# Optimization experiments

Hardware: AMD Instinct MI355X
Metric: run time of the kernel (lower is better)

## Reference

```python
import jax, jax.numpy as jnp
import numpy as np

N, B, E = 50000, 1, 800000
D_IN = 128      # input_size == out_size (residual)
HID = 128       # hidden_size
H = 4           # heads
C = HID // H    # per-head dim = 32
EPS = 1e-5


def setup_inputs() -> dict:
    key = jax.random.key(0)
    ks = jax.random.split(key, 16)
    s_in = 1.0 / np.sqrt(D_IN)
    s_hid = 1.0 / np.sqrt(HID)
    return {
        "x": jax.random.normal(ks[0], (N, B, D_IN), jnp.float32),
        "edge_index": jax.random.randint(ks[1], (2, E), 0, N, jnp.int64 if jax.config.jax_enable_x64 else jnp.int32),
        "edge_attr": jax.random.normal(ks[2], (E, HID), jnp.float32),
        # TransformerConv projections (weights stored torch-style [out, in])
        "Wq": jax.random.uniform(ks[3], (HID, D_IN), jnp.float32, -s_in, s_in),
        "bq": jnp.zeros((HID,), jnp.float32),
        "Wk": jax.random.uniform(ks[4], (HID, D_IN), jnp.float32, -s_in, s_in),
        "bk": jnp.zeros((HID,), jnp.float32),
        "Wv": jax.random.uniform(ks[5], (HID, D_IN), jnp.float32, -s_in, s_in),
        "bv": jnp.zeros((HID,), jnp.float32),
        "We": jax.random.uniform(ks[6], (HID, HID), jnp.float32, -s_hid, s_hid),  # lin_edge, no bias
        "Wskip": jax.random.uniform(ks[7], (HID, D_IN), jnp.float32, -s_in, s_in),
        "bskip": jnp.zeros((HID,), jnp.float32),
        "Wp": jax.random.uniform(ks[8], (HID, HID), jnp.float32, -s_hid, s_hid),   # physics_linear
        "bp": jnp.zeros((HID,), jnp.float32),
        "Wm": jax.random.uniform(ks[9], (D_IN, HID), jnp.float32, -s_hid, s_hid),  # merge_linear
        "bm": jnp.zeros((D_IN,), jnp.float32),
    }


def reference(x, edge_index, edge_attr, Wq, bq, Wk, bk, Wv, bv, We,
              Wskip, bskip, Wp, bp, Wm, bm):
    n = x.shape[0]
    src, dst = edge_index[0], edge_index[1]  # message flows src -> dst (j -> i)

    # node-wise QKV projections -> [N, B, H, C]
    q = (x @ Wq.T + bq).reshape(n, B, H, C)
    k = (x @ Wk.T + bk).reshape(n, B, H, C)
    v = (x @ Wv.T + bv).reshape(n, B, H, C)

    # edge feature projection -> [E, H, C]
    e = (edge_attr @ We.T).reshape(-1, H, C)

    # per-edge attention scores [E, B, H]
    k_j = k[src] + e[:, None]                       # [E, B, H, C]
    alpha = (q[dst] * k_j).sum(-1) / jnp.sqrt(jnp.asarray(C, x.dtype))

    # scatter-softmax over incoming edges of each dst node
    m = jax.ops.segment_max(alpha, dst, num_segments=n)      # [N, B, H]
    a = jnp.exp(alpha - m[dst])
    s = jax.ops.segment_sum(a, dst, num_segments=n)
    alpha = a / s[dst]

    # weighted scatter-add aggregation
    msg = (v[src] + e[:, None]) * alpha[..., None]           # [E, B, H, C]
    out = jax.ops.segment_sum(msg, dst, num_segments=n)      # [N, B, H, C]
    out = out.reshape(n, B, H * C)

    # root skip connection
    out = out + (x @ Wskip.T + bskip)

    # GraphResidualBlock tail
    out = jax.nn.relu(out)
    out = out @ Wp.T + bp
    # custom LayerNorm: normalize over the node dim (dim 0), weight/bias unused
    mu = out.mean(0, keepdims=True)
    sd = out.std(0, keepdims=True)
    out = (out - mu) / (sd + EPS)
    out = jax.nn.relu(out)
    out = out @ Wm.T + bm
    return out + x
```

## Files before the change

kernel.cpp:

```cpp
#include <hip/hip_runtime.h>
#include <stdint.h>

#define RS32 0.17677669529663687f
#define LDW 40

typedef short bf16x8 __attribute__((ext_vector_type(8)));
typedef float f32x4 __attribute__((ext_vector_type(4)));

__device__ __forceinline__ ushort f2bf(float f) {
  uint32_t b = __float_as_uint(f);
  b = (b + 0x7fffu + ((b >> 16) & 1u)) >> 16;
  return (ushort)b;
}
__device__ __forceinline__ float bflo(uint32_t w) { return __uint_as_float(w << 16); }
__device__ __forceinline__ float bfhi(uint32_t w) { return __uint_as_float(w & 0xffff0000u); }

__device__ __forceinline__ void stage16(ushort* hiA, ushort* loA, int r, int koff,
                                        const float* v) {
  uint32_t hu[8], lu[8];
#pragma unroll
  for (int i = 0; i < 8; ++i) {
    ushort h0 = f2bf(v[2 * i]), h1 = f2bf(v[2 * i + 1]);
    float f0 = __uint_as_float(((uint32_t)h0) << 16);
    float f1 = __uint_as_float(((uint32_t)h1) << 16);
    ushort l0 = f2bf(v[2 * i] - f0), l1 = f2bf(v[2 * i + 1] - f1);
    hu[i] = (uint32_t)h0 | ((uint32_t)h1 << 16);
    lu[i] = (uint32_t)l0 | ((uint32_t)l1 << 16);
  }
  *(uint4*)&hiA[r * LDW + koff]     = make_uint4(hu[0], hu[1], hu[2], hu[3]);
  *(uint4*)&hiA[r * LDW + koff + 8] = make_uint4(hu[4], hu[5], hu[6], hu[7]);
  *(uint4*)&loA[r * LDW + koff]     = make_uint4(lu[0], lu[1], lu[2], lu[3]);
  *(uint4*)&loA[r * LDW + koff + 8] = make_uint4(lu[4], lu[5], lu[6], lu[7]);
}

__launch_bounds__(256)
__global__ void gemm128_mfma_kernel(int mode,
                                    const float* __restrict__ A, const float* __restrict__ A2,
                                    const float* __restrict__ W, const float* __restrict__ bias,
                                    const float* __restrict__ mu, const float* __restrict__ inv,
                                    const float* __restrict__ X, float* __restrict__ out, int N)
{
  __shared__ ushort Ahi[128 * LDW], Alo[128 * LDW], Whi[128 * LDW], Wlo[128 * LDW];
  const int tid = threadIdx.x;
  const int nb = blockIdx.x * 128;
  const int lane = tid & 63, wv = tid >> 6;
  const int wr = (wv >> 1) * 64, wc = (wv & 1) * 64;
  const int fr = lane & 15, fq = lane >> 4;
  const int sr = tid >> 1, sk = (tid & 1) * 16;

  f32x4 acc[4][4];
#pragma unroll
  for (int m = 0; m < 4; ++m)
#pragma unroll
    for (int n = 0; n < 4; ++n) acc[m][n] = (f32x4)0.0f;

  for (int kc = 0; kc < 128; kc += 32) {
    float va[16], vw[16];
    {
      int gr = nb + sr;
      if (gr < N) {
#pragma unroll
        for (int i = 0; i < 4; ++i) {
          float4 v = *(const float4*)(A + (size_t)gr * 128 + kc + sk + i * 4);
          if (mode == 1) {
            float4 b = *(const float4*)(A2 + (size_t)gr * 128 + kc + sk + i * 4);
            v.x = fmaxf(v.x + b.x, 0.f); v.y = fmaxf(v.y + b.y, 0.f);
            v.z = fmaxf(v.z + b.z, 0.f); v.w = fmaxf(v.w + b.w, 0.f);
          } else if (mode == 2) {
            float4 m4 = *(const float4*)(mu + kc + sk + i * 4);
            float4 i4 = *(const float4*)(inv + kc + sk + i * 4);
            v.x = fmaxf((v.x - m4.x) * i4.x, 0.f); v.y = fmaxf((v.y - m4.y) * i4.y, 0.f);
            v.z = fmaxf((v.z - m4.z) * i4.z, 0.f); v.w = fmaxf((v.w - m4.w) * i4.w, 0.f);
          }
          va[i * 4 + 0] = v.x; va[i * 4 + 1] = v.y; va[i * 4 + 2] = v.z; va[i * 4 + 3] = v.w;
        }
      } else {
#pragma unroll
        for (int i = 0; i < 16; ++i) va[i] = 0.f;
      }
#pragma unroll
      for (int i = 0; i < 4; ++i) {
        float4 v = *(const float4*)(W + (size_t)sr * 128 + kc + sk + i * 4);
        vw[i * 4 + 0] = v.x; vw[i * 4 + 1] = v.y; vw[i * 4 + 2] = v.z; vw[i * 4 + 3] = v.w;
      }
    }
    if (kc) __syncthreads();
    stage16(Ahi, Alo, sr, sk, va);
    stage16(Whi, Wlo, sr, sk, vw);
    __syncthreads();

    bf16x8 ah[4], al[4], bh[4], bl[4];
#pragma unroll
    for (int m = 0; m < 4; ++m) {
      const int row = wr + m * 16 + fr;
      ah[m] = *(const bf16x8*)&Ahi[row * LDW + fq * 8];
      al[m] = *(const bf16x8*)&Alo[row * LDW + fq * 8];
    }
#pragma unroll
    for (int n = 0; n < 4; ++n) {
      const int col = wc + n * 16 + fr;
      bh[n] = *(const bf16x8*)&Whi[col * LDW + fq * 8];
      bl[n] = *(const bf16x8*)&Wlo[col * LDW + fq * 8];
    }
#pragma unroll
    for (int m = 0; m < 4; ++m)
#pragma unroll
      for (int n = 0; n < 4; ++n) {
        acc[m][n] = __builtin_amdgcn_mfma_f32_16x16x32_bf16(ah[m], bh[n], acc[m][n], 0, 0, 0);
        acc[m][n] = __builtin_amdgcn_mfma_f32_16x16x32_bf16(al[m], bh[n], acc[m][n], 0, 0, 0);
        acc[m][n] = __builtin_amdgcn_mfma_f32_16x16x32_bf16(ah[m], bl[n], acc[m][n], 0, 0, 0);
      }
  }

  float bcol[4];
#pragma unroll
  for (int n = 0; n < 4; ++n) bcol[n] = bias[wc + n * 16 + fr];
#pragma unroll
  for (int m = 0; m < 4; ++m) {
    const int r0 = nb + wr + m * 16 + fq * 4;
#pragma unroll
    for (int r = 0; r < 4; ++r) {
      const int gr = r0 + r;
      if (gr < N) {
#pragma unroll
        for (int n = 0; n < 4; ++n) {
          const int c = wc + n * 16 + fr;
          float o = acc[m][n][r] + bcol[n];
          if (mode == 2) o += X[(size_t)gr * 128 + c];
          out[(size_t)gr * 128 + c] = o;
        }
      }
    }
  }
}

__launch_bounds__(256)
__global__ void gemmqkvs_mfma_kernel(const float* __restrict__ x,
                                     const float* __restrict__ Wq, const float* __restrict__ bq,
                                     const float* __restrict__ Wk, const float* __restrict__ bk,
                                     const float* __restrict__ Wv, const float* __restrict__ bv,
                                     const float* __restrict__ Ws, const float* __restrict__ bs,
                                     float* __restrict__ oq, float* __restrict__ ok,
                                     float* __restrict__ ov, float* __restrict__ os, int N)
{
  const float* W; const float* bias; float* out;
  if (blockIdx.y == 0)      { W = Wq; bias = bq; out = oq; }
  else if (blockIdx.y == 1) { W = Wk; bias = bk; out = ok; }
  else if (blockIdx.y == 2) { W = Wv; bias = bv; out = ov; }
  else                      { W = Ws; bias = bs; out = os; }

  __shared__ ushort Ahi[128 * LDW], Alo[128 * LDW], Whi[128 * LDW], Wlo[128 * LDW];
  const int tid = threadIdx.x;
  const int nb = blockIdx.x * 128;
  const int lane = tid & 63, wv = tid >> 6;
  const int wr = (wv >> 1) * 64, wc = (wv & 1) * 64;
  const int fr = lane & 15, fq = lane >> 4;
  const int sr = tid >> 1, sk = (tid & 1) * 16;

  f32x4 acc[4][4];
#pragma unroll
  for (int m = 0; m < 4; ++m)
#pragma unroll
    for (int n = 0; n < 4; ++n) acc[m][n] = (f32x4)0.0f;

  for (int kc = 0; kc < 128; kc += 32) {
    float va[16], vw[16];
    {
      int gr = nb + sr;
      if (gr < N) {
#pragma unroll
        for (int i = 0; i < 4; ++i) {
          float4 v = *(const float4*)(x + (size_t)gr * 128 + kc + sk + i * 4);
          va[i * 4 + 0] = v.x; va[i * 4 + 1] = v.y; va[i * 4 + 2] = v.z; va[i * 4 + 3] = v.w;
        }
      } else {
#pragma unroll
        for (int i = 0; i < 16; ++i) va[i] = 0.f;
      }
#pragma unroll
      for (int i = 0; i < 4; ++i) {
        float4 v = *(const float4*)(W + (size_t)sr * 128 + kc + sk + i * 4);
        vw[i * 4 + 0] = v.x; vw[i * 4 + 1] = v.y; vw[i * 4 + 2] = v.z; vw[i * 4 + 3] = v.w;
      }
    }
    if (kc) __syncthreads();
    stage16(Ahi, Alo, sr, sk, va);
    stage16(Whi, Wlo, sr, sk, vw);
    __syncthreads();

    bf16x8 ah[4], al[4], bh[4], bl[4];
#pragma unroll
    for (int m = 0; m < 4; ++m) {
      const int row = wr + m * 16 + fr;
      ah[m] = *(const bf16x8*)&Ahi[row * LDW + fq * 8];
      al[m] = *(const bf16x8*)&Alo[row * LDW + fq * 8];
    }
#pragma unroll
    for (int n = 0; n < 4; ++n) {
      const int col = wc + n * 16 + fr;
      bh[n] = *(const bf16x8*)&Whi[col * LDW + fq * 8];
      bl[n] = *(const bf16x8*)&Wlo[col * LDW + fq * 8];
    }
#pragma unroll
    for (int m = 0; m < 4; ++m)
#pragma unroll
      for (int n = 0; n < 4; ++n) {
        acc[m][n] = __builtin_amdgcn_mfma_f32_16x16x32_bf16(ah[m], bh[n], acc[m][n], 0, 0, 0);
        acc[m][n] = __builtin_amdgcn_mfma_f32_16x16x32_bf16(al[m], bh[n], acc[m][n], 0, 0, 0);
        acc[m][n] = __builtin_amdgcn_mfma_f32_16x16x32_bf16(ah[m], bl[n], acc[m][n], 0, 0, 0);
      }
  }

  float bcol[4];
#pragma unroll
  for (int n = 0; n < 4; ++n) bcol[n] = bias[wc + n * 16 + fr];
#pragma unroll
  for (int m = 0; m < 4; ++m) {
    const int r0 = nb + wr + m * 16 + fq * 4;
#pragma unroll
    for (int r = 0; r < 4; ++r) {
      const int gr = r0 + r;
      if (gr < N) {
#pragma unroll
        for (int n = 0; n < 4; ++n) {
          const int c = wc + n * 16 + fr;
          out[(size_t)gr * 128 + c] = acc[m][n][r] + bcol[n];
        }
      }
    }
  }
}

__launch_bounds__(256)
__global__ void u_kernel(const float* __restrict__ q, const float* __restrict__ We,
                         ushort* __restrict__ u, int N)
{
  __shared__ float qs[64][128];
  const int tid = threadIdx.x;
  const int nb = blockIdx.x * 64;
  for (int idx = tid; idx < 64 * 128; idx += 256) {
    int r = idx >> 7, kk = idx & 127;
    qs[r][kk] = (nb + r < N) ? q[(size_t)(nb + r) * 128 + kk] : 0.f;
  }
  __syncthreads();
  const int j = tid & 127, half = tid >> 7;
  for (int h = 0; h < 4; ++h) {
    float w[32];
#pragma unroll
    for (int c = 0; c < 32; ++c) w[c] = We[(size_t)(32 * h + c) * 128 + j];
    for (int nn = half; nn < 64; nn += 2) {
      float acc = 0.f;
#pragma unroll
      for (int c4 = 0; c4 < 32; c4 += 4) {
        float4 qq = *(const float4*)&qs[nn][32 * h + c4];
        acc = fmaf(qq.x, w[c4], acc);
        acc = fmaf(qq.y, w[c4 + 1], acc);
        acc = fmaf(qq.z, w[c4 + 2], acc);
        acc = fmaf(qq.w, w[c4 + 3], acc);
      }
      int gr = nb + nn;
      if (gr < N) u[(size_t)gr * 512 + h * 128 + j] = f2bf(acc);
    }
  }
}

__global__ void prep_web_kernel(const float* __restrict__ We, ushort* __restrict__ WeB)
{
  int idx = blockIdx.x * 256 + threadIdx.x;
  if (idx >= 128 * 512) return;
  int c = idx >> 9, j = idx & 511;
  int hh = j >> 7, k2 = j & 127;
  WeB[idx] = (hh == (c >> 5)) ? f2bf(We[(size_t)c * 128 + k2]) : (ushort)0;
}

__global__ void deg_kernel(const int* __restrict__ ei, int* __restrict__ deg, int E)
{
  int e = blockIdx.x * 256 + threadIdx.x;
  if (e < E) atomicAdd(&deg[ei[E + e]], 1);
}

__launch_bounds__(256)
__global__ void start_kernel(const int* __restrict__ deg, int* __restrict__ offs,
                             int* __restrict__ cursor, int* __restrict__ gcount, int N)
{
  const int i = blockIdx.x * 256 + threadIdx.x;
  const int lane = threadIdx.x & 63;
  int d = (i < N) ? deg[i] : 0;
  int scan = d;
#pragma unroll
  for (int ofs = 1; ofs < 64; ofs <<= 1) {
    int t = __shfl_up(scan, ofs, 64);
    if (lane >= ofs) scan += t;
  }
  int total = __shfl(scan, 63, 64);
  int base = 0;
  if (lane == 63) base = atomicAdd(gcount, total);
  base = __shfl(base, 63, 64);
  int excl = base + scan - d;
  if (i < N) { offs[i] = excl; cursor[i] = excl; }
}

__global__ void fill_kernel(const int* __restrict__ ei, int* __restrict__ cursor,
                            int2* __restrict__ csr, int E)
{
  int e = blockIdx.x * 256 + threadIdx.x;
  if (e < E) {
    int dst = ei[E + e];
    int slot = atomicAdd(&cursor[dst], 1);
    csr[slot] = make_int2(ei[e], e);
  }
}

__launch_bounds__(256)
__global__ void fused_attn2_kernel(const int2* __restrict__ csr, const int* __restrict__ offs,
                                   const int* __restrict__ deg,
                                   const float* __restrict__ q, const float* __restrict__ kbuf,
                                   const float* __restrict__ vbuf, const ushort* __restrict__ u,
                                   const float* __restrict__ eattr,
                                   ushort* __restrict__ aggS, float* __restrict__ wsS, int N)
{
  const int tid = threadIdx.x;
  const int lane = tid & 63;
  const int wid = tid >> 6;
  const int p = lane >> 5;
  const int j32 = lane & 31;
  const int c0 = j32 * 4;
  const int h = j32 >> 3;
  const int gwave = blockIdx.x * 4 + wid;
  const int nwaves = gridDim.x * 4;

  for (int n = gwave; n < N; n += nwaves) {
    const int e0 = offs[n];
    const int e1 = e0 + deg[n];

    const float4 qv = *(const float4*)(q + (size_t)n * 128 + c0);
    float uh[4][4];
#pragma unroll
    for (int hh = 0; hh < 4; ++hh) {
      uint2 U = *(const uint2*)(u + (size_t)n * 512 + hh * 128 + c0);
      uh[hh][0] = bflo(U.x); uh[hh][1] = bfhi(U.x);
      uh[hh][2] = bflo(U.y); uh[hh][3] = bfhi(U.y);
    }

    float ws0 = 0.f, ws1 = 0.f, ws2 = 0.f, ws3 = 0.f;
    float ax[4][4];
#pragma unroll
    for (int hh = 0; hh < 4; ++hh)
#pragma unroll
      for (int j = 0; j < 4; ++j) ax[hh][j] = 0.f;
    float sm0 = 0.f, sm1 = 0.f, sm2 = 0.f, sm3 = 0.f;

    int sl = e0 + p;
    if (sl < e1) {
      int2 seC = csr[sl];
      float4 eaC = *(const float4*)(eattr + (size_t)seC.y * 128 + c0);
      float4 kC  = *(const float4*)(kbuf + (size_t)seC.x * 128 + c0);
      float4 vC  = *(const float4*)(vbuf + (size_t)seC.x * 128 + c0);
      int sln = sl + 2;
      int2 seN = (sln < e1) ? csr[sln] : seC;
      for (; sl < e1; sl += 2) {
        float4 eaN = *(const float4*)(eattr + (size_t)seN.y * 128 + c0);
        float4 kN  = *(const float4*)(kbuf + (size_t)seN.x * 128 + c0);
        float4 vN  = *(const float4*)(vbuf + (size_t)seN.x * 128 + c0);
        const int slf = sl + 4;
        int2 seF = (slf < e1) ? csr[slf] : seN;

        float P0 = eaC.x * uh[0][0] + eaC.y * uh[0][1] + eaC.z * uh[0][2] + eaC.w * uh[0][3];
        float P1 = eaC.x * uh[1][0] + eaC.y * uh[1][1] + eaC.z * uh[1][2] + eaC.w * uh[1][3];
        float P2 = eaC.x * uh[2][0] + eaC.y * uh[2][1] + eaC.z * uh[2][2] + eaC.w * uh[2][3];
        float P3 = eaC.x * uh[3][0] + eaC.y * uh[3][1] + eaC.z * uh[3][2] + eaC.w * uh[3][3];
        const float qk = qv.x * kC.x + qv.y * kC.y + qv.z * kC.z + qv.w * kC.w;
        P0 += (h == 0) ? qk : 0.f;
        P1 += (h == 1) ? qk : 0.f;
        P2 += (h == 2) ? qk : 0.f;
        P3 += (h == 3) ? qk : 0.f;
#pragma unroll
        for (int mm = 1; mm <= 16; mm <<= 1) {
          P0 += __shfl_xor(P0, mm, 64);
          P1 += __shfl_xor(P1, mm, 64);
          P2 += __shfl_xor(P2, mm, 64);
          P3 += __shfl_xor(P3, mm, 64);
        }
        const float a0 = __expf(P0 * RS32);
        const float a1 = __expf(P1 * RS32);
        const float a2 = __expf(P2 * RS32);
        const float a3 = __expf(P3 * RS32);
        sm0 += a0; sm1 += a1; sm2 += a2; sm3 += a3;
        const float aV = (h == 0) ? a0 : (h == 1) ? a1 : (h == 2) ? a2 : a3;
        ws0 = fmaf(aV, vC.x, ws0); ws1 = fmaf(aV, vC.y, ws1);
        ws2 = fmaf(aV, vC.z, ws2); ws3 = fmaf(aV, vC.w, ws3);
        ax[0][0] = fmaf(a0, eaC.x, ax[0][0]); ax[0][1] = fmaf(a0, eaC.y, ax[0][1]);
        ax[0][2] = fmaf(a0, eaC.z, ax[0][2]); ax[0][3] = fmaf(a0, eaC.w, ax[0][3]);
        ax[1][0] = fmaf(a1, eaC.x, ax[1][0]); ax[1][1] = fmaf(a1, eaC.y, ax[1][1]);
        ax[1][2] = fmaf(a1, eaC.z, ax[1][2]); ax[1][3] = fmaf(a1, eaC.w, ax[1][3]);
        ax[2][0] = fmaf(a2, eaC.x, ax[2][0]); ax[2][1] = fmaf(a2, eaC.y, ax[2][1]);
        ax[2][2] = fmaf(a2, eaC.z, ax[2][2]); ax[2][3] = fmaf(a2, eaC.w, ax[2][3]);
        ax[3][0] = fmaf(a3, eaC.x, ax[3][0]); ax[3][1] = fmaf(a3, eaC.y, ax[3][1]);
        ax[3][2] = fmaf(a3, eaC.z, ax[3][2]); ax[3][3] = fmaf(a3, eaC.w, ax[3][3]);

        eaC = eaN; kC = kN; vC = vN; seN = seF;
      }
    }

#pragma unroll
    for (int hh = 0; hh < 4; ++hh)
#pragma unroll
      for (int j = 0; j < 4; ++j) ax[hh][j] += __shfl_xor(ax[hh][j], 32, 64);
    ws0 += __shfl_xor(ws0, 32, 64); ws1 += __shfl_xor(ws1, 32, 64);
    ws2 += __shfl_xor(ws2, 32, 64); ws3 += __shfl_xor(ws3, 32, 64);
    sm0 += __shfl_xor(sm0, 32, 64); sm1 += __shfl_xor(sm1, 32, 64);
    sm2 += __shfl_xor(sm2, 32, 64); sm3 += __shfl_xor(sm3, 32, 64);

    const float iv0 = (sm0 > 0.f) ? 1.f / sm0 : 0.f;
    const float iv1 = (sm1 > 0.f) ? 1.f / sm1 : 0.f;
    const float iv2 = (sm2 > 0.f) ? 1.f / sm2 : 0.f;
    const float iv3 = (sm3 > 0.f) ? 1.f / sm3 : 0.f;

    if (p == 0) {
      const float s = (h == 0) ? iv0 : (h == 1) ? iv1 : (h == 2) ? iv2 : iv3;
      *(float4*)(wsS + (size_t)n * 128 + c0) =
          make_float4(ws0 * s, ws1 * s, ws2 * s, ws3 * s);
    }

    float o0[4], o1[4], s0, s1;
    if (p == 0) {
#pragma unroll
      for (int j = 0; j < 4; ++j) { o0[j] = ax[0][j]; o1[j] = ax[1][j]; }
      s0 = iv0; s1 = iv1;
    } else {
#pragma unroll
      for (int j = 0; j < 4; ++j) { o0[j] = ax[2][j]; o1[j] = ax[3][j]; }
      s0 = iv2; s1 = iv3;
    }
    uint2 w0 = make_uint2(((uint32_t)f2bf(o0[0] * s0)) | (((uint32_t)f2bf(o0[1] * s0)) << 16),
                          ((uint32_t)f2bf(o0[2] * s0)) | (((uint32_t)f2bf(o0[3] * s0)) << 16));
    uint2 w1 = make_uint2(((uint32_t)f2bf(o1[0] * s1)) | (((uint32_t)f2bf(o1[1] * s1)) << 16),
                          ((uint32_t)f2bf(o1[2] * s1)) | (((uint32_t)f2bf(o1[3] * s1)) << 16));
    *(uint2*)(aggS + (size_t)n * 512 + (p * 2) * 128 + c0) = w0;
    *(uint2*)(aggS + (size_t)n * 512 + (p * 2 + 1) * 128 + c0) = w1;
  }
}

__launch_bounds__(256)
__global__ void agg_gemm_kernel(const ushort* __restrict__ aggS, const ushort* __restrict__ WeB,
                                const float* __restrict__ wsX, float* __restrict__ attn, int N)
{
  __shared__ ushort As[128][72];
  __shared__ ushort Bs[128][72];
  const int tid = threadIdx.x;
  const int nb = blockIdx.x * 128;
  const int lane = tid & 63, wv = tid >> 6;
  const int wr = (wv >> 1) * 64, wc = (wv & 1) * 64;
  const int fr = lane & 15, fq = lane >> 4;
  const int r = tid >> 1, cs = (tid & 1) * 32;

  f32x4 acc[4][4];
#pragma unroll
  for (int m = 0; m < 4; ++m)
#pragma unroll
    for (int n = 0; n < 4; ++n) acc[m][n] = (f32x4)0.0f;

  for (int kc = 0; kc < 512; kc += 64) {
    uint4 av[4], bv[4];
    if (nb + r < N) {
      const uint4* src = (const uint4*)(aggS + (size_t)(nb + r) * 512 + kc + cs);
      av[0] = src[0]; av[1] = src[1]; av[2] = src[2]; av[3] = src[3];
    } else {
#pragma unroll
      for (int i = 0; i < 4; ++i) av[i] = make_uint4(0, 0, 0, 0);
    }
    {
      const uint4* src = (const uint4*)(WeB + (size_t)r * 512 + kc + cs);
      bv[0] = src[0]; bv[1] = src[1]; bv[2] = src[2]; bv[3] = src[3];
    }
    if (kc) __syncthreads();
#pragma unroll
    for (int i = 0; i < 4; ++i) {
      *(uint4*)&As[r][cs + i * 8] = av[i];
      *(uint4*)&Bs[r][cs + i * 8] = bv[i];
    }
    __syncthreads();

#pragma unroll
    for (int s = 0; s < 2; ++s) {
      bf16x8 ah[4], bh[4];
#pragma unroll
      for (int m = 0; m < 4; ++m)
        ah[m] = *(const bf16x8*)&As[wr + m * 16 + fr][s * 32 + fq * 8];
#pragma unroll
      for (int n = 0; n < 4; ++n)
        bh[n] = *(const bf16x8*)&Bs[wc + n * 16 + fr][s * 32 + fq * 8];
#pragma unroll
      for (int m = 0; m < 4; ++m)
#pragma unroll
        for (int n = 0; n < 4; ++n)
          acc[m][n] = __builtin_amdgcn_mfma_f32_16x16x32_bf16(ah[m], bh[n], acc[m][n], 0, 0, 0);
    }
  }

#pragma unroll
  for (int m = 0; m < 4; ++m) {
    const int r0 = nb + wr + m * 16 + fq * 4;
#pragma unroll
    for (int rr = 0; rr < 4; ++rr) {
      const int gr = r0 + rr;
      if (gr < N) {
#pragma unroll
        for (int n = 0; n < 4; ++n) {
          const int c = wc + n * 16 + fr;
          attn[(size_t)gr * 128 + c] = acc[m][n][rr] + wsX[(size_t)gr * 128 + c];
        }
      }
    }
  }
}

__launch_bounds__(256)
__global__ void stats_kernel(const float* __restrict__ t1, float* __restrict__ sums,
                             float* __restrict__ sumsq, int N)
{
  const int tid = threadIdx.x;
  const int c = tid & 127, half = tid >> 7;
  float s = 0.f, s2 = 0.f;
  for (int r = blockIdx.x * 2 + half; r < N; r += gridDim.x * 2) {
    float vv = t1[(size_t)r * 128 + c];
    s += vv; s2 = fmaf(vv, vv, s2);
  }
  __shared__ float ls[256], ls2[256];
  ls[tid] = s; ls2[tid] = s2;
  __syncthreads();
  if (tid < 128) {
    atomicAdd(&sums[c], ls[tid] + ls[tid + 128]);
    atomicAdd(&sumsq[c], ls2[tid] + ls2[tid + 128]);
  }
}

__global__ void finalize_stats_kernel(const float* __restrict__ sums, const float* __restrict__ sumsq,
                                      float* __restrict__ mu, float* __restrict__ inv, int N)
{
  int c = threadIdx.x;
  float m = sums[c] / (float)N;
  float var = sumsq[c] / (float)N - m * m;
  float sd = sqrtf(fmaxf(var, 0.f));
  mu[c] = m;
  inv[c] = 1.f / (sd + 1e-5f);
}

extern "C" void kernel_launch(void* const* d_in, const int* in_sizes, int n_in,
                              void* d_out, int out_size, void* d_ws, size_t ws_size,
                              hipStream_t stream) {
  const float* x    = (const float*)d_in[0];
  const int*   ei   = (const int*)d_in[1];
  const float* eatt = (const float*)d_in[2];
  const float* Wq = (const float*)d_in[3];  const float* bq = (const float*)d_in[4];
  const float* Wk = (const float*)d_in[5];  const float* bk = (const float*)d_in[6];
  const float* Wv = (const float*)d_in[7];  const float* bv = (const float*)d_in[8];
  const float* We = (const float*)d_in[9];
  const float* Wsk = (const float*)d_in[10]; const float* bsk = (const float*)d_in[11];
  const float* Wp = (const float*)d_in[12]; const float* bp = (const float*)d_in[13];
  const float* Wm = (const float*)d_in[14]; const float* bm = (const float*)d_in[15];
  float* out = (float*)d_out;

  const int N = in_sizes[0] / 128;
  const int E = in_sizes[1] / 2;

  char* w = (char*)d_ws;
  auto alloc = [&](size_t bytes) {
    char* p = w;
    w += (bytes + 255) & ~(size_t)255;
    return p;
  };
  const size_t node_f = (size_t)N * 128 * sizeof(float);
  float*  q    = (float*)alloc(node_f);
  float*  kk   = (float*)alloc(node_f);
  float*  vv   = (float*)alloc(node_f);
  float*  skip = (float*)alloc(node_f);
  float*  wsA  = (float*)alloc(node_f);
  ushort* u    = (ushort*)alloc((size_t)N * 512 * sizeof(ushort));
  ushort* aggS = (ushort*)alloc((size_t)N * 512 * sizeof(ushort));
  ushort* WeB  = (ushort*)alloc(128 * 512 * sizeof(ushort));
  int*    deg  = (int*)alloc((size_t)N * sizeof(int));
  int*    offs = (int*)alloc((size_t)N * sizeof(int));
  int*    curs = (int*)alloc((size_t)N * sizeof(int));
  int*    gcnt = (int*)alloc(sizeof(int));
  int2*   csr  = (int2*)alloc((size_t)E * sizeof(int2));
  float*  sums  = (float*)alloc(128 * sizeof(float));
  float*  sumsq = (float*)alloc(128 * sizeof(float));
  float*  mu    = (float*)alloc(128 * sizeof(float));
  float*  inv   = (float*)alloc(128 * sizeof(float));
  float*  t1   = q;
  (void)ws_size; (void)n_in; (void)out_size;

  const int NB = (N + 127) / 128;
  const int EB = (E + 255) / 256;

  hipMemsetAsync(deg, 0, (size_t)N * sizeof(int), stream);
  hipMemsetAsync(gcnt, 0, sizeof(int), stream);
  hipMemsetAsync(sums, 0, 2 * 128 * sizeof(float), stream);

  gemmqkvs_mfma_kernel<<<dim3(NB, 4), 256, 0, stream>>>(x, Wq, bq, Wk, bk, Wv, bv, Wsk, bsk,
                                                        q, kk, vv, skip, N);
  u_kernel<<<(N + 63) / 64, 256, 0, stream>>>(q, We, u, N);
  prep_web_kernel<<<256, 256, 0, stream>>>(We, WeB);

  deg_kernel<<<EB, 256, 0, stream>>>(ei, deg, E);
  start_kernel<<<(N + 255) / 256, 256, 0, stream>>>(deg, offs, curs, gcnt, N);
  fill_kernel<<<EB, 256, 0, stream>>>(ei, curs, csr, E);

  fused_attn2_kernel<<<2048, 256, 0, stream>>>(csr, offs, deg, q, kk, vv, u, eatt,
                                               aggS, wsA, N);

  agg_gemm_kernel<<<NB, 256, 0, stream>>>(aggS, WeB, wsA, wsA, N);

  gemm128_mfma_kernel<<<NB, 256, 0, stream>>>(1, wsA, skip, Wp, bp, nullptr, nullptr, nullptr, t1, N);

  stats_kernel<<<256, 256, 0, stream>>>(t1, sums, sumsq, N);
  finalize_stats_kernel<<<1, 128, 0, stream>>>(sums, sumsq, mu, inv, N);

  gemm128_mfma_kernel<<<NB, 256, 0, stream>>>(2, t1, nullptr, Wm, bm, mu, inv, x, out, N);
}
```

Measured before the change: 559.1 us.

## Store K/V as interleaved bf16 and fuse column stats into physics GEMM

The QKV projection kernel now writes K and V as bf16 into one interleaved per-node buffer, so the edge-gather loop in the attention kernel fetches half as many bytes per source node and reads K and V from the same row. The separate stats pass over t1 is removed. Column sums and sums of squares are accumulated in the epilogue of the physics GEMM, reduced with wave shuffles and added with atomics. This lowers gather bandwidth and drops one full read of t1, at the cost of bf16 rounding error in the attention scores and values, plus many more atomics on 128 addresses.

```diff
diff --git a/kernel.cpp b/kernel.cpp
--- a/kernel.cpp
+++ b/kernel.cpp
@@ -38,7 +38,8 @@
                                     const float* __restrict__ A, const float* __restrict__ A2,
                                     const float* __restrict__ W, const float* __restrict__ bias,
                                     const float* __restrict__ mu, const float* __restrict__ inv,
-                                    const float* __restrict__ X, float* __restrict__ out, int N)
+                                    const float* __restrict__ X, float* __restrict__ out,
+                                    float* __restrict__ sums, float* __restrict__ sumsq, int N)
 {
   __shared__ ushort Ahi[128 * LDW], Alo[128 * LDW], Whi[128 * LDW], Wlo[128 * LDW];
   const int tid = threadIdx.x;
@@ -115,6 +116,7 @@
   float bcol[4];
 #pragma unroll
   for (int n = 0; n < 4; ++n) bcol[n] = bias[wc + n * 16 + fr];
+  float csum[4] = {0.f, 0.f, 0.f, 0.f}, csum2[4] = {0.f, 0.f, 0.f, 0.f};
 #pragma unroll
   for (int m = 0; m < 4; ++m) {
     const int r0 = nb + wr + m * 16 + fq * 4;
@@ -128,7 +130,24 @@
           float o = acc[m][n][r] + bcol[n];
           if (mode == 2) o += X[(size_t)gr * 128 + c];
           out[(size_t)gr * 128 + c] = o;
+          if (mode == 1) { csum[n] += o; csum2[n] = fmaf(o, o, csum2[n]); }
         }
+      }
+    }
+  }
+  if (mode == 1) {
+#pragma unroll
+    for (int n = 0; n < 4; ++n) {
+      csum[n] += __shfl_xor(csum[n], 16, 64);
+      csum[n] += __shfl_xor(csum[n], 32, 64);
+      csum2[n] += __shfl_xor(csum2[n], 16, 64);
+      csum2[n] += __shfl_xor(csum2[n], 32, 64);
+    }
+    if (fq == 0) {
+#pragma unroll
+      for (int n = 0; n < 4; ++n) {
+        atomicAdd(&sums[wc + n * 16 + fr], csum[n]);
+        atomicAdd(&sumsq[wc + n * 16 + fr], csum2[n]);
       }
     }
   }
@@ -140,14 +159,14 @@
                                      const float* __restrict__ Wk, const float* __restrict__ bk,
                                      const float* __restrict__ Wv, const float* __restrict__ bv,
                                      const float* __restrict__ Ws, const float* __restrict__ bs,
-                                     float* __restrict__ oq, float* __restrict__ ok,
-                                     float* __restrict__ ov, float* __restrict__ os, int N)
-{
-  const float* W; const float* bias; float* out;
-  if (blockIdx.y == 0)      { W = Wq; bias = bq; out = oq; }
-  else if (blockIdx.y == 1) { W = Wk; bias = bk; out = ok; }
-  else if (blockIdx.y == 2) { W = Wv; bias = bv; out = ov; }
-  else                      { W = Ws; bias = bs; out = os; }
+                                     float* __restrict__ oq, float* __restrict__ os,
+                                     ushort* __restrict__ kvb, int N)
+{
+  const float* W; const float* bias;
+  if (blockIdx.y == 0)      { W = Wq; bias = bq; }
+  else if (blockIdx.y == 1) { W = Wk; bias = bk; }
+  else if (blockIdx.y == 2) { W = Wv; bias = bv; }
+  else                      { W = Ws; bias = bs; }
 
   __shared__ ushort Ahi[128 * LDW], Alo[128 * LDW], Whi[128 * LDW], Wlo[128 * LDW];
   const int tid = threadIdx.x;
@@ -214,6 +233,9 @@
   float bcol[4];
 #pragma unroll
   for (int n = 0; n < 4; ++n) bcol[n] = bias[wc + n * 16 + fr];
+  const int y = blockIdx.y;
+  float* outf = (y == 0) ? oq : os;
+  const int voff = (y == 2) ? 128 : 0;
 #pragma unroll
   for (int m = 0; m < 4; ++m) {
     const int r0 = nb + wr + m * 16 + fq * 4;
@@ -224,7 +246,9 @@
 #pragma unroll
         for (int n = 0; n < 4; ++n) {
           const int c = wc + n * 16 + fr;
-          out[(size_t)gr * 128 + c] = acc[m][n][r] + bcol[n];
+          float o = acc[m][n][r] + bcol[n];
+          if (y == 0 || y == 3) outf[(size_t)gr * 128 + c] = o;
+          else kvb[(size_t)gr * 256 + voff + c] = f2bf(o);
         }
       }
     }
@@ -314,8 +338,8 @@
 __launch_bounds__(256)
 __global__ void fused_attn2_kernel(const int2* __restrict__ csr, const int* __restrict__ offs,
                                    const int* __restrict__ deg,
-                                   const float* __restrict__ q, const float* __restrict__ kbuf,
-                                   const float* __restrict__ vbuf, const ushort* __restrict__ u,
+                                   const float* __restrict__ q, const ushort* __restrict__ kvb,
+                                   const ushort* __restrict__ u,
                                    const float* __restrict__ eattr,
                                    ushort* __restrict__ aggS, float* __restrict__ wsS, int N)
 {
@@ -354,22 +378,25 @@
     if (sl < e1) {
       int2 seC = csr[sl];
       float4 eaC = *(const float4*)(eattr + (size_t)seC.y * 128 + c0);
-      float4 kC  = *(const float4*)(kbuf + (size_t)seC.x * 128 + c0);
-      float4 vC  = *(const float4*)(vbuf + (size_t)seC.x * 128 + c0);
+      uint2 kC = *(const uint2*)(kvb + (size_t)seC.x * 256 + c0);
+      uint2 vC = *(const uint2*)(kvb + (size_t)seC.x * 256 + 128 + c0);
       int sln = sl + 2;
       int2 seN = (sln < e1) ? csr[sln] : seC;
       for (; sl < e1; sl += 2) {
         float4 eaN = *(const float4*)(eattr + (size_t)seN.y * 128 + c0);
-        float4 kN  = *(const float4*)(kbuf + (size_t)seN.x * 128 + c0);
-        float4 vN  = *(const float4*)(vbuf + (size_t)seN.x * 128 + c0);
+        uint2 kN = *(const uint2*)(kvb + (size_t)seN.x * 256 + c0);
+        uint2 vN = *(const uint2*)(kvb + (size_t)seN.x * 256 + 128 + c0);
         const int slf = sl + 4;
         int2 seF = (slf < e1) ? csr[slf] : seN;
+
+        const float kf0 = bflo(kC.x), kf1 = bfhi(kC.x), kf2 = bflo(kC.y), kf3 = bfhi(kC.y);
+        const float vf0 = bflo(vC.x), vf1 = bfhi(vC.x), vf2 = bflo(vC.y), vf3 = bfhi(vC.y);
 
         float P0 = eaC.x * uh[0][0] + eaC.y * uh[0][1] + eaC.z * uh[0][2] + eaC.w * uh[0][3];
         float P1 = eaC.x * uh[1][0] + eaC.y * uh[1][1] + eaC.z * uh[1][2] + eaC.w * uh[1][3];
         float P2 = eaC.x * uh[2][0] + eaC.y * uh[2][1] + eaC.z * uh[2][2] + eaC.w * uh[2][3];
         float P3 = eaC.x * uh[3][0] + eaC.y * uh[3][1] + eaC.z * uh[3][2] + eaC.w * uh[3][3];
-        const float qk = qv.x * kC.x + qv.y * kC.y + qv.z * kC.z + qv.w * kC.w;
+        const float qk = qv.x * kf0 + qv.y * kf1 + qv.z * kf2 + qv.w * kf3;
         P0 += (h == 0) ? qk : 0.f;
         P1 += (h == 1) ? qk : 0.f;
         P2 += (h == 2) ? qk : 0.f;
@@ -387,8 +414,8 @@
         const float a3 = __expf(P3 * RS32);
         sm0 += a0; sm1 += a1; sm2 += a2; sm3 += a3;
         const float aV = (h == 0) ? a0 : (h == 1) ? a1 : (h == 2) ? a2 : a3;
-        ws0 = fmaf(aV, vC.x, ws0); ws1 = fmaf(aV, vC.y, ws1);
-        ws2 = fmaf(aV, vC.z, ws2); ws3 = fmaf(aV, vC.w, ws3);
+        ws0 = fmaf(aV, vf0, ws0); ws1 = fmaf(aV, vf1, ws1);
+        ws2 = fmaf(aV, vf2, ws2); ws3 = fmaf(aV, vf3, ws3);
         ax[0][0] = fmaf(a0, eaC.x, ax[0][0]); ax[0][1] = fmaf(a0, eaC.y, ax[0][1]);
         ax[0][2] = fmaf(a0, eaC.z, ax[0][2]); ax[0][3] = fmaf(a0, eaC.w, ax[0][3]);
         ax[1][0] = fmaf(a1, eaC.x, ax[1][0]); ax[1][1] = fmaf(a1, eaC.y, ax[1][1]);
@@ -512,26 +539,6 @@
         }
       }
     }
-  }
-}
-
-__launch_bounds__(256)
-__global__ void stats_kernel(const float* __restrict__ t1, float* __restrict__ sums,
-                             float* __restrict__ sumsq, int N)
-{
-  const int tid = threadIdx.x;
-  const int c = tid & 127, half = tid >> 7;
-  float s = 0.f, s2 = 0.f;
-  for (int r = blockIdx.x * 2 + half; r < N; r += gridDim.x * 2) {
-    float vv = t1[(size_t)r * 128 + c];
-    s += vv; s2 = fmaf(vv, vv, s2);
-  }
-  __shared__ float ls[256], ls2[256];
-  ls[tid] = s; ls2[tid] = s2;
-  __syncthreads();
-  if (tid < 128) {
-    atomicAdd(&sums[c], ls[tid] + ls[tid + 128]);
-    atomicAdd(&sumsq[c], ls2[tid] + ls2[tid + 128]);
   }
 }
 
@@ -572,10 +579,9 @@
   };
   const size_t node_f = (size_t)N * 128 * sizeof(float);
   float*  q    = (float*)alloc(node_f);
-  float*  kk   = (float*)alloc(node_f);
-  float*  vv   = (float*)alloc(node_f);
   float*  skip = (float*)alloc(node_f);
   float*  wsA  = (float*)alloc(node_f);
+  ushort* kvb  = (ushort*)alloc((size_t)N * 256 * sizeof(ushort));
   ushort* u    = (ushort*)alloc((size_t)N * 512 * sizeof(ushort));
   ushort* aggS = (ushort*)alloc((size_t)N * 512 * sizeof(ushort));
   ushort* WeB  = (ushort*)alloc(128 * 512 * sizeof(ushort));
@@ -599,7 +605,7 @@
   hipMemsetAsync(sums, 0, 2 * 128 * sizeof(float), stream);
 
   gemmqkvs_mfma_kernel<<<dim3(NB, 4), 256, 0, stream>>>(x, Wq, bq, Wk, bk, Wv, bv, Wsk, bsk,
-                                                        q, kk, vv, skip, N);
+                                                        q, skip, kvb, N);
   u_kernel<<<(N + 63) / 64, 256, 0, stream>>>(q, We, u, N);
   prep_web_kernel<<<256, 256, 0, stream>>>(We, WeB);
 
@@ -607,15 +613,15 @@
   start_kernel<<<(N + 255) / 256, 256, 0, stream>>>(deg, offs, curs, gcnt, N);
   fill_kernel<<<EB, 256, 0, stream>>>(ei, curs, csr, E);
 
-  fused_attn2_kernel<<<2048, 256, 0, stream>>>(csr, offs, deg, q, kk, vv, u, eatt,
+  fused_attn2_kernel<<<2048, 256, 0, stream>>>(csr, offs, deg, q, kvb, u, eatt,
                                                aggS, wsA, N);
 
   agg_gemm_kernel<<<NB, 256, 0, stream>>>(aggS, WeB, wsA, wsA, N);
 
-  gemm128_mfma_kernel<<<NB, 256, 0, stream>>>(1, wsA, skip, Wp, bp, nullptr, nullptr, nullptr, t1, N);
-
-  stats_kernel<<<256, 256, 0, stream>>>(t1, sums, sumsq, N);
+  gemm128_mfma_kernel<<<NB, 256, 0, stream>>>(1, wsA, skip, Wp, bp, nullptr, nullptr, nullptr,
+                                              t1, sums, sumsq, N);
   finalize_stats_kernel<<<1, 128, 0, stream>>>(sums, sumsq, mu, inv, N);
 
-  gemm128_mfma_kernel<<<NB, 256, 0, stream>>>(2, t1, nullptr, Wm, bm, mu, inv, x, out, N);
-}
+  gemm128_mfma_kernel<<<NB, 256, 0, stream>>>(2, t1, nullptr, Wm, bm, mu, inv, x, out,
+                                              nullptr, nullptr, N);
+}
```

Result: faster. 512.5 us (-8.3%).
